# Performance work log

Measured on AMD Instinct MI355X. Metric: run time of the kernel, lower is better.

The kernel has to match this reference:

```python
import jax, jax.numpy as jnp
import numpy as np

N_NODES = 100000
N_EDGES = 800000
D_IN = 128
D_EDGE = 128
D_OUT = 128


def setup_inputs() -> dict:
    key = jax.random.key(0)
    ks = jax.random.split(key, 8)
    return {
        "nfeats": jax.random.normal(ks[0], (N_NODES, D_IN), dtype=jnp.float32),
        "efeats": jax.random.normal(ks[1], (N_EDGES, D_EDGE), dtype=jnp.float32),
        "src": jax.random.randint(ks[2], (N_EDGES,), 0, N_NODES, dtype=jnp.int32),
        "dst": jax.random.randint(ks[3], (N_EDGES,), 0, N_NODES, dtype=jnp.int32),
        "W_msg_w": jax.random.normal(ks[4], (D_OUT, D_IN + D_EDGE), dtype=jnp.float32) * 0.05,
        "W_msg_b": jax.random.normal(ks[5], (D_OUT,), dtype=jnp.float32) * 0.05,
        "W_apply_w": jax.random.normal(ks[6], (D_OUT, D_IN + D_OUT), dtype=jnp.float32) * 0.05,
        "W_apply_b": jax.random.normal(ks[7], (D_OUT,), dtype=jnp.float32) * 0.05,
    }


def reference(nfeats, efeats, src, dst, W_msg_w, W_msg_b, W_apply_w, W_apply_b):
    N = nfeats.shape[0]
    # unsqueeze(1): [N,1,din], [E,1,dedge] (batch-of-1 middle dim, as in the torch code)
    h = nfeats[:, None, :]
    e = efeats[:, None, :]
    # message: W_msg(cat(src_h, edge_h))  -> [E,1,dout]
    msg_in = jnp.concatenate([h[src], e], axis=2)
    msg = jnp.einsum('ebi,oi->ebo', msg_in, W_msg_w) + W_msg_b
    # mean-aggregate messages by destination node (DGL fn.mean; empty -> 0)
    agg = jax.ops.segment_sum(msg, dst, num_segments=N)  # [N,1,dout]
    deg = jax.ops.segment_sum(jnp.ones((dst.shape[0],), msg.dtype), dst, num_segments=N)  # [N]
    h_neigh = agg / jnp.maximum(deg, 1.0)[:, None, None]
    # node update: relu(W_apply(cat(h, h_neigh)))
    upd_in = jnp.concatenate([h, h_neigh], axis=2)  # [N,1,din+dout]
    new_h = jax.nn.relu(jnp.einsum('nbi,oi->nbo', upd_in, W_apply_w) + W_apply_b)
    # edge update: average of endpoint embeddings
    new_e = (new_h[src] + new_h[dst]) * 0.5  # [E,1,dout]
    return new_h, new_e
```

## Files before the change

kernel.cpp:

```cpp
#include <hip/hip_runtime.h>

#define D 128

typedef __attribute__((ext_vector_type(4))) float f32x4;
typedef __attribute__((ext_vector_type(8))) short s16x8;

__device__ inline unsigned short f2bf(float x){
  unsigned u = __builtin_bit_cast(unsigned, x);
  u += 0x7FFFu + ((u>>16)&1u);
  return (unsigned short)(u>>16);
}
__device__ inline float bf2f(unsigned short u){
  return __builtin_bit_cast(float, (unsigned)u << 16);
}

__device__ inline void gload_lds16(const void* g, void* l){
  __builtin_amdgcn_global_load_lds(
      (const __attribute__((address_space(1))) void*)g,
      (__attribute__((address_space(3))) void*)l, 16, 0, 0);
}

__global__ void k_hist(const int* __restrict__ dst, int* __restrict__ counts, int E){
  int e = blockIdx.x*256 + threadIdx.x;
  if (e < E) atomicAdd(&counts[dst[e]], 1);
}

__global__ void k_scan1(const int* __restrict__ counts, int* __restrict__ partials, int N){
  __shared__ int sd[256];
  int t = threadIdx.x;
  int base = blockIdx.x*1024 + t*4;
  int s = 0;
  #pragma unroll
  for (int j=0;j<4;j++){ int i=base+j; s += (i<N)?counts[i]:0; }
  sd[t]=s; __syncthreads();
  for (int off=128; off>0; off>>=1){ if (t<off) sd[t]+=sd[t+off]; __syncthreads(); }
  if (t==0) partials[blockIdx.x]=sd[0];
}

__global__ void k_scan2(int* __restrict__ partials, int* __restrict__ row_ptr, int nb, int N){
  __shared__ int sd[1024];
  int t = threadIdx.x;
  if (nb <= 1024){
    int v = (t < nb) ? partials[t] : 0;
    sd[t] = v;
    __syncthreads();
    #pragma unroll
    for (int off=1; off<1024; off<<=1){
      int x = (t >= off) ? sd[t-off] : 0;
      __syncthreads();
      sd[t] += x;
      __syncthreads();
    }
    if (t < nb) partials[t] = sd[t] - v;
    if (t == 1023) row_ptr[N] = sd[1023];
  } else if (t == 0){
    int run=0;
    for (int b=0;b<nb;b++){ int v=partials[b]; partials[b]=run; run+=v; }
    row_ptr[N]=run;
  }
}

__global__ void k_scan3(const int* __restrict__ counts, const int* __restrict__ partials,
                        int* __restrict__ row_ptr, int* __restrict__ cursor, int N){
  __shared__ int sd[256];
  int t=threadIdx.x;
  int base = blockIdx.x*1024 + t*4;
  int v[4]; int s=0;
  #pragma unroll
  for (int j=0;j<4;j++){ int i=base+j; v[j]=(i<N)?counts[i]:0; s+=v[j]; }
  sd[t]=s; __syncthreads();
  for (int off=1; off<256; off<<=1){
    int x = (t>=off)? sd[t-off] : 0;
    __syncthreads();
    sd[t] += x;
    __syncthreads();
  }
  int run = sd[t]-s + partials[blockIdx.x];
  #pragma unroll
  for (int j=0;j<4;j++){ int i=base+j; if (i<N){ row_ptr[i]=run; cursor[i]=run; } run+=v[j]; }
}

__global__ void k_scatter(const int* __restrict__ src, const int* __restrict__ dst,
                          int* __restrict__ cursor, int2* __restrict__ es, int E){
  int e = blockIdx.x*256+threadIdx.x;
  if (e<E){
    int d = dst[e];
    int p = atomicAdd(&cursor[d],1);
    int2 v; v.x = e; v.y = src[e];
    es[p] = v;
  }
}

__global__ void k_cvt(const float* __restrict__ in, unsigned short* __restrict__ out, int n8){
  int i = blockIdx.x*256 + threadIdx.x;
  if (i >= n8) return;
  const float4* p = reinterpret_cast<const float4*>(in) + (size_t)i*2;
  float4 a = p[0], b = p[1];
  union { unsigned short s[8]; uint4 u; } r;
  r.s[0]=f2bf(a.x); r.s[1]=f2bf(a.y); r.s[2]=f2bf(a.z); r.s[3]=f2bf(a.w);
  r.s[4]=f2bf(b.x); r.s[5]=f2bf(b.y); r.s[6]=f2bf(b.z); r.s[7]=f2bf(b.w);
  reinterpret_cast<uint4*>(out)[i] = r.u;
}

__global__ void k_comb(const float* __restrict__ Wa, const float* __restrict__ Wm,
                       const float* __restrict__ bm, unsigned short* __restrict__ Mbf,
                       float* __restrict__ Wb){
  int o = blockIdx.x; int t = threadIdx.x;
  if (t < 128){
    Mbf[o*384+t] = f2bf(Wa[o*256+t]);
  } else {
    int i = t-128;
    float s=0.f;
    #pragma unroll 4
    for (int p=0;p<128;p++) s += Wa[o*256+128+p]*Wm[p*256+i];
    Mbf[o*384+t] = f2bf(s);
  }
  if (t==0){
    float s=0.f;
    for (int p=0;p<128;p++) s += Wa[o*256+128+p]*bm[p];
    Wb[o]=s;
  }
}

__global__ void k_agg(const unsigned short* __restrict__ nfb, const float* __restrict__ ef,
                      const int* __restrict__ rp, const int2* __restrict__ es,
                      unsigned short* __restrict__ Sbf, float* __restrict__ flagA, int N){
  int n = blockIdx.x*4 + (threadIdx.x>>6);
  int lane = threadIdx.x & 63;
  if (n>=N) return;
  int r0 = rp[n], r1 = rp[n+1];
  float dinv = 1.0f/fmaxf((float)(r1-r0),1.0f);
  float aH0=0.f,aH1=0.f,aE0=0.f,aE1=0.f;
  int j = r0;
  for (; j+4<=r1; j+=4){
    int2 p0=es[j], p1=es[j+1], p2=es[j+2], p3=es[j+3];
    ushort2 h0 = reinterpret_cast<const ushort2*>(nfb + (size_t)p0.y*D)[lane];
    ushort2 h1 = reinterpret_cast<const ushort2*>(nfb + (size_t)p1.y*D)[lane];
    ushort2 h2 = reinterpret_cast<const ushort2*>(nfb + (size_t)p2.y*D)[lane];
    ushort2 h3 = reinterpret_cast<const ushort2*>(nfb + (size_t)p3.y*D)[lane];
    float2 e0 = reinterpret_cast<const float2*>(ef + (size_t)p0.x*D)[lane];
    float2 e1 = reinterpret_cast<const float2*>(ef + (size_t)p1.x*D)[lane];
    float2 e2 = reinterpret_cast<const float2*>(ef + (size_t)p2.x*D)[lane];
    float2 e3 = reinterpret_cast<const float2*>(ef + (size_t)p3.x*D)[lane];
    aH0 += (bf2f(h0.x)+bf2f(h1.x))+(bf2f(h2.x)+bf2f(h3.x));
    aH1 += (bf2f(h0.y)+bf2f(h1.y))+(bf2f(h2.y)+bf2f(h3.y));
    aE0 += (e0.x+e1.x)+(e2.x+e3.x);
    aE1 += (e0.y+e1.y)+(e2.y+e3.y);
  }
  for (; j<r1; j++){
    int2 p = es[j];
    ushort2 h = reinterpret_cast<const ushort2*>(nfb + (size_t)p.y*D)[lane];
    float2 e2 = reinterpret_cast<const float2*>(ef + (size_t)p.x*D)[lane];
    aH0+=bf2f(h.x); aH1+=bf2f(h.y); aE0+=e2.x; aE1+=e2.y;
  }
  ushort2* So = reinterpret_cast<ushort2*>(Sbf + (size_t)n*256);
  ushort2 th; th.x = f2bf(aH0*dinv); th.y = f2bf(aH1*dinv);
  ushort2 te; te.x = f2bf(aE0*dinv); te.y = f2bf(aE1*dinv);
  So[lane]    = th;
  So[64+lane] = te;
  if (lane==0) flagA[n] = (r1>r0) ? 1.0f : 0.0f;
}

__global__ __launch_bounds__(256) void k_gemm(
    const unsigned short* __restrict__ nfb, const unsigned short* __restrict__ Sbf,
    const unsigned short* __restrict__ Mbf, const float* __restrict__ ba,
    const float* __restrict__ Wb, const float* __restrict__ flagA,
    float* __restrict__ outH, unsigned short* __restrict__ Hb, int N)
{
  __shared__ __align__(16) unsigned short As[128*32];
  __shared__ __align__(16) unsigned short Bs[128*32];
  int tid = threadIdx.x;
  int lane = tid & 63;
  int w = tid >> 6;
  int wr = w >> 1, wc = w & 1;
  int bn = blockIdx.x * 128;

  f32x4 acc[4][4];
  #pragma unroll
  for (int i=0;i<4;i++)
    #pragma unroll
    for (int j=0;j<4;j++) acc[i][j] = (f32x4){0.f,0.f,0.f,0.f};

  int lr = lane >> 2;
  int lb = (lane & 3) * 16;

  for (int kb = 0; kb < 384; kb += 32){
    #pragma unroll
    for (int c = 0; c < 2; c++){
      int rbase = w*32 + c*16;
      int row = rbase + lr;
      int n = bn + row; if (n >= N) n = N-1;
      const char* g;
      if (kb < 128) g = (const char*)nfb + (size_t)n*256 + (size_t)kb*2 + lb;
      else          g = (const char*)Sbf + (size_t)n*512 + (size_t)(kb-128)*2 + lb;
      gload_lds16(g, &As[rbase*32]);
      const char* gm = (const char*)Mbf + (size_t)row*768 + (size_t)kb*2 + lb;
      gload_lds16(gm, &Bs[rbase*32]);
    }
    __syncthreads();
    s16x8 af[4], bfr[4];
    int kg = (lane>>4)*8;
    #pragma unroll
    for (int bi=0;bi<4;bi++)
      af[bi] = *reinterpret_cast<const s16x8*>(&As[(wr*64 + bi*16 + (lane&15))*32 + kg]);
    #pragma unroll
    for (int bj=0;bj<4;bj++)
      bfr[bj] = *reinterpret_cast<const s16x8*>(&Bs[(wc*64 + bj*16 + (lane&15))*32 + kg]);
    #pragma unroll
    for (int bi=0;bi<4;bi++)
      #pragma unroll
      for (int bj=0;bj<4;bj++)
        acc[bi][bj] = __builtin_amdgcn_mfma_f32_16x16x32_bf16(af[bi], bfr[bj], acc[bi][bj], 0, 0, 0);
    __syncthreads();
  }

  float bav[4], wbv[4];
  #pragma unroll
  for (int bj=0;bj<4;bj++){
    int col = wc*64 + bj*16 + (lane&15);
    bav[bj] = ba[col]; wbv[bj] = Wb[col];
  }
  #pragma unroll
  for (int bi=0;bi<4;bi++){
    int rb = bn + wr*64 + bi*16 + (lane>>4)*4;
    #pragma unroll
    for (int r=0;r<4;r++){
      int row = rb + r;
      if (row < N){
        float fl = flagA[row];
        #pragma unroll
        for (int bj=0;bj<4;bj++){
          int col = wc*64 + bj*16 + (lane&15);
          float v = fmaxf(acc[bi][bj][r] + bav[bj] + fl*wbv[bj], 0.f);
          outH[(size_t)row*128 + col] = v;
          Hb[(size_t)row*128 + col] = f2bf(v);
        }
      }
    }
  }
}

__global__ void k_edge_csr(const unsigned short* __restrict__ Hb, const int* __restrict__ rp,
                           const int2* __restrict__ es, float* __restrict__ NE, int N){
  int n = blockIdx.x*4 + (threadIdx.x>>6);
  if (n>=N) return;
  int lane = threadIdx.x & 63;
  int half = lane >> 5, l = lane & 31;
  int r0 = rp[n], r1 = rp[n+1];
  const ushort4* H4 = reinterpret_cast<const ushort4*>(Hb);
  float4* NE4 = reinterpret_cast<float4*>(NE);
  ushort4 hnu = H4[(size_t)n*32 + l];
  float4 hn = make_float4(bf2f(hnu.x), bf2f(hnu.y), bf2f(hnu.z), bf2f(hnu.w));
  int j = r0;
  for (; j+4<=r1; j+=4){
    int2 p0 = es[j+half], p1 = es[j+2+half];
    ushort4 u0 = H4[(size_t)p0.y*32 + l];
    ushort4 u1 = H4[(size_t)p1.y*32 + l];
    float4 o0, o1;
    o0.x=0.5f*(hn.x+bf2f(u0.x)); o0.y=0.5f*(hn.y+bf2f(u0.y));
    o0.z=0.5f*(hn.z+bf2f(u0.z)); o0.w=0.5f*(hn.w+bf2f(u0.w));
    o1.x=0.5f*(hn.x+bf2f(u1.x)); o1.y=0.5f*(hn.y+bf2f(u1.y));
    o1.z=0.5f*(hn.z+bf2f(u1.z)); o1.w=0.5f*(hn.w+bf2f(u1.w));
    NE4[(size_t)p0.x*32 + l] = o0;
    NE4[(size_t)p1.x*32 + l] = o1;
  }
  if (j+2<=r1){
    int2 p = es[j+half];
    ushort4 u = H4[(size_t)p.y*32 + l];
    float4 o;
    o.x=0.5f*(hn.x+bf2f(u.x)); o.y=0.5f*(hn.y+bf2f(u.y));
    o.z=0.5f*(hn.z+bf2f(u.z)); o.w=0.5f*(hn.w+bf2f(u.w));
    NE4[(size_t)p.x*32 + l] = o;
    j += 2;
  }
  if (j<r1 && half==0){
    int2 p = es[j];
    ushort4 u = H4[(size_t)p.y*32 + l];
    float4 o;
    o.x=0.5f*(hn.x+bf2f(u.x)); o.y=0.5f*(hn.y+bf2f(u.y));
    o.z=0.5f*(hn.z+bf2f(u.z)); o.w=0.5f*(hn.w+bf2f(u.w));
    NE4[(size_t)p.x*32 + l] = o;
  }
}

__global__ void k_edge(const int* __restrict__ src, const int* __restrict__ dst,
                       const float* __restrict__ H, float* __restrict__ NE, int E){
  int t = threadIdx.x;
  int e = blockIdx.x*8 + (t>>5);
  if (e>=E) return;
  int l = t & 31;
  const float4* Hs = reinterpret_cast<const float4*>(H + (size_t)src[e]*D);
  const float4* Hd = reinterpret_cast<const float4*>(H + (size_t)dst[e]*D);
  float4 a = Hs[l], b = Hd[l];
  float4 r;
  r.x = 0.5f*(a.x+b.x); r.y = 0.5f*(a.y+b.y);
  r.z = 0.5f*(a.z+b.z); r.w = 0.5f*(a.w+b.w);
  reinterpret_cast<float4*>(NE + (size_t)e*D)[l] = r;
}

extern "C" void kernel_launch(void* const* d_in, const int* in_sizes, int n_in,
                              void* d_out, int out_size, void* d_ws, size_t ws_size,
                              hipStream_t stream)
{
  const float* nf  = (const float*)d_in[0];
  const float* ef  = (const float*)d_in[1];
  const int*   src = (const int*)d_in[2];
  const int*   dst = (const int*)d_in[3];
  const float* Wm  = (const float*)d_in[4];
  const float* bm  = (const float*)d_in[5];
  const float* Wa  = (const float*)d_in[6];
  const float* bap = (const float*)d_in[7];
  int N = in_sizes[0]/D;
  int E = in_sizes[2];
  float* outH = (float*)d_out;
  float* outE = (float*)d_out + (size_t)N*D;

  size_t off = 0;
  auto alloc = [&](size_t bytes){ size_t o = off; off = (off + bytes + 255) & ~(size_t)255; return o; };
  size_t o_counts = alloc((size_t)N*4);
  size_t o_rp     = alloc((size_t)(N+1)*4);
  size_t o_part   = alloc(1024*4);
  size_t o_cur    = alloc((size_t)N*4);
  size_t o_es     = alloc((size_t)E*8);
  size_t o_M      = alloc((size_t)128*384*2);
  size_t o_wb     = alloc(128*4);
  size_t o_S      = alloc((size_t)N*256*2);
  size_t o_nfb    = alloc((size_t)N*128*2);
  size_t o_flag   = alloc((size_t)N*4);
  size_t o_hb     = alloc((size_t)N*128*2);
  size_t need = off;
  bool ws_ok = (ws_size >= need);
  char* base = ws_ok ? (char*)d_ws : (char*)(void*)outE;

  int* counts  = (int*)(base + o_counts);
  int* row_ptr = (int*)(base + o_rp);
  int* partials= (int*)(base + o_part);
  int* cursor  = (int*)(base + o_cur);
  int2* es     = (int2*)(base + o_es);
  unsigned short* Mbf = (unsigned short*)(base + o_M);
  float* Wb    = (float*)(base + o_wb);
  unsigned short* Sbf = (unsigned short*)(base + o_S);
  unsigned short* nfb = (unsigned short*)(base + o_nfb);
  float* flagA = (float*)(base + o_flag);
  unsigned short* Hb  = (unsigned short*)(base + o_hb);

  hipMemsetAsync(counts, 0, (size_t)N*4, stream);

  int NB = (N + 1023)/1024;
  k_hist   <<<(E+255)/256, 256, 0, stream>>>(dst, counts, E);
  k_scan1  <<<NB, 256, 0, stream>>>(counts, partials, N);
  k_scan2  <<<1, 1024, 0, stream>>>(partials, row_ptr, NB, N);
  k_scan3  <<<NB, 256, 0, stream>>>(counts, partials, row_ptr, cursor, N);
  k_scatter<<<(E+255)/256, 256, 0, stream>>>(src, dst, cursor, es, E);
  k_comb   <<<128, 384, 0, stream>>>(Wa, Wm, bm, Mbf, Wb);
  k_cvt    <<<(N*16 + 255)/256, 256, 0, stream>>>(nf, nfb, N*16);
  k_agg    <<<(N+3)/4, 256, 0, stream>>>(nfb, ef, row_ptr, es, Sbf, flagA, N);
  k_gemm   <<<(N+127)/128, 256, 0, stream>>>(nfb, Sbf, Mbf, bap, Wb, flagA, outH, Hb, N);
  if (ws_ok)
    k_edge_csr<<<(N+3)/4, 256, 0, stream>>>(Hb, row_ptr, es, outE, N);
  else
    k_edge    <<<(E+7)/8, 256, 0, stream>>>(src, dst, outH, outE, E);
}
```

Measured before the change: 415.4 us.

## Merge histogram, conversion and weight-combine into one launch; unroll gather loops by eight

Folds the degree histogram, node-feature bf16 conversion and weight-combination kernels into a single launch that picks its role from the block index, removing two kernel launches and their serialization gaps. The aggregation and edge-output loops now handle eight edges per iteration, issuing more independent gathers before any use so more memory requests are in flight. This costs extra registers, which may lower occupancy, and the wider unroll only helps nodes with degree of eight or more.

```diff
diff --git a/kernel.cpp b/kernel.cpp
--- a/kernel.cpp
+++ b/kernel.cpp
@@ -20,9 +20,43 @@
       (__attribute__((address_space(3))) void*)l, 16, 0, 0);
 }
 
-__global__ void k_hist(const int* __restrict__ dst, int* __restrict__ counts, int E){
-  int e = blockIdx.x*256 + threadIdx.x;
-  if (e < E) atomicAdd(&counts[dst[e]], 1);
+__global__ void k_pre(const int* __restrict__ dst, int* __restrict__ counts,
+                      const float* __restrict__ nf, unsigned short* __restrict__ nfb,
+                      const float* __restrict__ Wa, const float* __restrict__ Wm,
+                      const float* __restrict__ bm, unsigned short* __restrict__ Mbf,
+                      float* __restrict__ Wb,
+                      int E, int n8, int nbHist, int nbCvt){
+  int b = blockIdx.x, t = threadIdx.x;
+  if (b < nbHist){
+    int e = b*384 + t;
+    if (e < E) atomicAdd(&counts[dst[e]], 1);
+  } else if (b < nbHist + nbCvt){
+    int i = (b - nbHist)*384 + t;
+    if (i < n8){
+      const float4* p = reinterpret_cast<const float4*>(nf) + (size_t)i*2;
+      float4 a = p[0], bb = p[1];
+      union { unsigned short s[8]; uint4 u; } r;
+      r.s[0]=f2bf(a.x); r.s[1]=f2bf(a.y); r.s[2]=f2bf(a.z); r.s[3]=f2bf(a.w);
+      r.s[4]=f2bf(bb.x); r.s[5]=f2bf(bb.y); r.s[6]=f2bf(bb.z); r.s[7]=f2bf(bb.w);
+      reinterpret_cast<uint4*>(nfb)[i] = r.u;
+    }
+  } else {
+    int o = b - nbHist - nbCvt;
+    if (t < 128){
+      Mbf[o*384+t] = f2bf(Wa[o*256+t]);
+    } else {
+      int i = t-128;
+      float s=0.f;
+      #pragma unroll 4
+      for (int p=0;p<128;p++) s += Wa[o*256+128+p]*Wm[p*256+i];
+      Mbf[o*384+t] = f2bf(s);
+    }
+    if (t==0){
+      float s=0.f;
+      for (int p=0;p<128;p++) s += Wa[o*256+128+p]*bm[p];
+      Wb[o]=s;
+    }
+  }
 }
 
 __global__ void k_scan1(const int* __restrict__ counts, int* __restrict__ partials, int N){
@@ -88,37 +122,6 @@
     int p = atomicAdd(&cursor[d],1);
     int2 v; v.x = e; v.y = src[e];
     es[p] = v;
-  }
-}
-
-__global__ void k_cvt(const float* __restrict__ in, unsigned short* __restrict__ out, int n8){
-  int i = blockIdx.x*256 + threadIdx.x;
-  if (i >= n8) return;
-  const float4* p = reinterpret_cast<const float4*>(in) + (size_t)i*2;
-  float4 a = p[0], b = p[1];
-  union { unsigned short s[8]; uint4 u; } r;
-  r.s[0]=f2bf(a.x); r.s[1]=f2bf(a.y); r.s[2]=f2bf(a.z); r.s[3]=f2bf(a.w);
-  r.s[4]=f2bf(b.x); r.s[5]=f2bf(b.y); r.s[6]=f2bf(b.z); r.s[7]=f2bf(b.w);
-  reinterpret_cast<uint4*>(out)[i] = r.u;
-}
-
-__global__ void k_comb(const float* __restrict__ Wa, const float* __restrict__ Wm,
-                       const float* __restrict__ bm, unsigned short* __restrict__ Mbf,
-                       float* __restrict__ Wb){
-  int o = blockIdx.x; int t = threadIdx.x;
-  if (t < 128){
-    Mbf[o*384+t] = f2bf(Wa[o*256+t]);
-  } else {
-    int i = t-128;
-    float s=0.f;
-    #pragma unroll 4
-    for (int p=0;p<128;p++) s += Wa[o*256+128+p]*Wm[p*256+i];
-    Mbf[o*384+t] = f2bf(s);
-  }
-  if (t==0){
-    float s=0.f;
-    for (int p=0;p<128;p++) s += Wa[o*256+128+p]*bm[p];
-    Wb[o]=s;
   }
 }
 
@@ -132,6 +135,21 @@
   float dinv = 1.0f/fmaxf((float)(r1-r0),1.0f);
   float aH0=0.f,aH1=0.f,aE0=0.f,aE1=0.f;
   int j = r0;
+  for (; j+8<=r1; j+=8){
+    int2 p[8];
+    #pragma unroll
+    for (int q=0;q<8;q++) p[q] = es[j+q];
+    ushort2 h[8]; float2 e2[8];
+    #pragma unroll
+    for (int q=0;q<8;q++) h[q]  = reinterpret_cast<const ushort2*>(nfb + (size_t)p[q].y*D)[lane];
+    #pragma unroll
+    for (int q=0;q<8;q++) e2[q] = reinterpret_cast<const float2*>(ef  + (size_t)p[q].x*D)[lane];
+    #pragma unroll
+    for (int q=0;q<8;q++){
+      aH0 += bf2f(h[q].x); aH1 += bf2f(h[q].y);
+      aE0 += e2[q].x;      aE1 += e2[q].y;
+    }
+  }
   for (; j+4<=r1; j+=4){
     int2 p0=es[j], p1=es[j+1], p2=es[j+2], p3=es[j+3];
     ushort2 h0 = reinterpret_cast<const ushort2*>(nfb + (size_t)p0.y*D)[lane];
@@ -252,17 +270,38 @@
   ushort4 hnu = H4[(size_t)n*32 + l];
   float4 hn = make_float4(bf2f(hnu.x), bf2f(hnu.y), bf2f(hnu.z), bf2f(hnu.w));
   int j = r0;
-  for (; j+4<=r1; j+=4){
+  for (; j+8<=r1; j+=8){
+    int2 p0 = es[j+half], p1 = es[j+2+half], p2 = es[j+4+half], p3 = es[j+6+half];
+    ushort4 u0 = H4[(size_t)p0.y*32 + l];
+    ushort4 u1 = H4[(size_t)p1.y*32 + l];
+    ushort4 u2 = H4[(size_t)p2.y*32 + l];
+    ushort4 u3 = H4[(size_t)p3.y*32 + l];
+    float4 o;
+    o.x=0.5f*(hn.x+bf2f(u0.x)); o.y=0.5f*(hn.y+bf2f(u0.y));
+    o.z=0.5f*(hn.z+bf2f(u0.z)); o.w=0.5f*(hn.w+bf2f(u0.w));
+    NE4[(size_t)p0.x*32 + l] = o;
+    o.x=0.5f*(hn.x+bf2f(u1.x)); o.y=0.5f*(hn.y+bf2f(u1.y));
+    o.z=0.5f*(hn.z+bf2f(u1.z)); o.w=0.5f*(hn.w+bf2f(u1.w));
+    NE4[(size_t)p1.x*32 + l] = o;
+    o.x=0.5f*(hn.x+bf2f(u2.x)); o.y=0.5f*(hn.y+bf2f(u2.y));
+    o.z=0.5f*(hn.z+bf2f(u2.z)); o.w=0.5f*(hn.w+bf2f(u2.w));
+    NE4[(size_t)p2.x*32 + l] = o;
+    o.x=0.5f*(hn.x+bf2f(u3.x)); o.y=0.5f*(hn.y+bf2f(u3.y));
+    o.z=0.5f*(hn.z+bf2f(u3.z)); o.w=0.5f*(hn.w+bf2f(u3.w));
+    NE4[(size_t)p3.x*32 + l] = o;
+  }
+  if (j+4<=r1){
     int2 p0 = es[j+half], p1 = es[j+2+half];
     ushort4 u0 = H4[(size_t)p0.y*32 + l];
     ushort4 u1 = H4[(size_t)p1.y*32 + l];
-    float4 o0, o1;
-    o0.x=0.5f*(hn.x+bf2f(u0.x)); o0.y=0.5f*(hn.y+bf2f(u0.y));
-    o0.z=0.5f*(hn.z+bf2f(u0.z)); o0.w=0.5f*(hn.w+bf2f(u0.w));
-    o1.x=0.5f*(hn.x+bf2f(u1.x)); o1.y=0.5f*(hn.y+bf2f(u1.y));
-    o1.z=0.5f*(hn.z+bf2f(u1.z)); o1.w=0.5f*(hn.w+bf2f(u1.w));
-    NE4[(size_t)p0.x*32 + l] = o0;
-    NE4[(size_t)p1.x*32 + l] = o1;
+    float4 o;
+    o.x=0.5f*(hn.x+bf2f(u0.x)); o.y=0.5f*(hn.y+bf2f(u0.y));
+    o.z=0.5f*(hn.z+bf2f(u0.z)); o.w=0.5f*(hn.w+bf2f(u0.w));
+    NE4[(size_t)p0.x*32 + l] = o;
+    o.x=0.5f*(hn.x+bf2f(u1.x)); o.y=0.5f*(hn.y+bf2f(u1.y));
+    o.z=0.5f*(hn.z+bf2f(u1.z)); o.w=0.5f*(hn.w+bf2f(u1.w));
+    NE4[(size_t)p1.x*32 + l] = o;
+    j += 4;
   }
   if (j+2<=r1){
     int2 p = es[j+half];
@@ -346,14 +385,15 @@
 
   hipMemsetAsync(counts, 0, (size_t)N*4, stream);
 
+  int n8 = N*16;
+  int nbHist = (E + 383)/384;
+  int nbCvt  = (n8 + 383)/384;
   int NB = (N + 1023)/1024;
-  k_hist   <<<(E+255)/256, 256, 0, stream>>>(dst, counts, E);
+  k_pre    <<<nbHist + nbCvt + 128, 384, 0, stream>>>(dst, counts, nf, nfb, Wa, Wm, bm, Mbf, Wb, E, n8, nbHist, nbCvt);
   k_scan1  <<<NB, 256, 0, stream>>>(counts, partials, N);
   k_scan2  <<<1, 1024, 0, stream>>>(partials, row_ptr, NB, N);
   k_scan3  <<<NB, 256, 0, stream>>>(counts, partials, row_ptr, cursor, N);
   k_scatter<<<(E+255)/256, 256, 0, stream>>>(src, dst, cursor, es, E);
-  k_comb   <<<128, 384, 0, stream>>>(Wa, Wm, bm, Mbf, Wb);
-  k_cvt    <<<(N*16 + 255)/256, 256, 0, stream>>>(nf, nfb, N*16);
   k_agg    <<<(N+3)/4, 256, 0, stream>>>(nfb, ef, row_ptr, es, Sbf, flagA, N);
   k_gemm   <<<(N+127)/128, 256, 0, stream>>>(nfb, Sbf, Mbf, bap, Wb, flagA, outH, Hb, N);
   if (ws_ok)
```

After: 406.4 us. 2.2% less time.
